# Performance work log

Measured on AMD Instinct MI355X. Metric: run time of the kernel, lower is better.

The kernel has to match this reference:

```python
import jax, jax.numpy as jnp
import numpy as np

B, S, D, H, E, K = 1, 2048, 1024, 16, 8, 2
DK = D // H          # 64 per-head key dim
FF = 4 * D           # 4096 expert hidden
EPS = 1e-5


def rmsnorm(x, scale):
    rms = jnp.sqrt(jnp.mean(x * x, axis=-1, keepdims=True) + EPS)
    return scale * (x / rms)


def setup_inputs() -> dict:
    key = jax.random.key(0)
    ks = jax.random.split(key, 12)
    std = 0.02
    x = jax.random.normal(ks[0], (B, S, D), dtype=jnp.float32)
    # causal mask: masked_fill where mask == 0
    self_attn_mask = jnp.tril(jnp.ones((S, S), dtype=jnp.int32))
    scale_attn = jnp.ones((D,), dtype=jnp.float32)
    scale_ffn = jnp.ones((D,), dtype=jnp.float32)
    # per-head projections, stacked: [H, DK, D] (torch Linear weight layout [out,in])
    Wq = jax.random.normal(ks[1], (H, DK, D), dtype=jnp.float32) * std
    Wk = jax.random.normal(ks[2], (H, DK, D), dtype=jnp.float32) * std
    Wv = jax.random.normal(ks[3], (H, DK, D), dtype=jnp.float32) * std
    Wo = jax.random.normal(ks[4], (D, D), dtype=jnp.float32) * std
    Wg = jax.random.normal(ks[5], (E, D), dtype=jnp.float32) * std   # router gate
    W_in = jax.random.normal(ks[6], (E, FF, D), dtype=jnp.float32) * std   # expert linear
    W_v = jax.random.normal(ks[7], (E, FF, D), dtype=jnp.float32) * std    # expert linear_v
    W_out = jax.random.normal(ks[8], (E, D, FF), dtype=jnp.float32) * std  # expert linear_out
    return {
        'x': x, 'self_attn_mask': self_attn_mask,
        'scale_attn': scale_attn, 'Wq': Wq, 'Wk': Wk, 'Wv': Wv, 'Wo': Wo,
        'scale_ffn': scale_ffn, 'Wg': Wg, 'W_in': W_in, 'W_v': W_v, 'W_out': W_out,
    }


def reference(x, self_attn_mask, scale_attn, Wq, Wk, Wv, Wo, scale_ffn, Wg, W_in, W_v, W_out):
    # --- self attention (pre-RMSNorm) ---
    normed = rmsnorm(x, scale_attn)
    q = jnp.einsum('bsd,hkd->bhsk', normed, Wq)
    k = jnp.einsum('bsd,hkd->bhsk', normed, Wk)
    v = jnp.einsum('bsd,hkd->bhsk', normed, Wv)
    attn = jnp.einsum('bhsk,bhtk->bhst', q, k) / np.sqrt(DK).astype(np.float32)
    attn = jnp.where(self_attn_mask[None, None] == 0, -jnp.inf, attn)
    attn = jax.nn.softmax(attn, axis=-1)
    ctx = jnp.einsum('bhst,bhtk->bhsk', attn, v)
    ctx = ctx.transpose(0, 2, 1, 3).reshape(x.shape[0], x.shape[1], D)  # concat heads
    a1 = ctx @ Wo.T
    x = x + a1
    # --- MoE (pre-RMSNorm) ---
    normed = rmsnorm(x, scale_ffn)
    router_logits = normed @ Wg.T                       # [B,S,E]
    router_probs = jax.nn.softmax(router_logits, axis=-1)
    gate, idx = jax.lax.top_k(router_probs, K)          # [B,S,K]
    gate = gate / jnp.sum(gate, axis=-1, keepdims=True)
    # combine weights per expert: sum of renormalized gates over selected slots
    onehot = (idx[..., None] == jnp.arange(E)).astype(x.dtype)  # [B,S,K,E]
    combine = jnp.sum(gate[..., None] * onehot, axis=2)         # [B,S,E]
    # all-expert dense FFN (faithful to the masked dense loop in torch)
    g = jax.nn.gelu(jnp.einsum('bsd,efd->bsef', normed, W_in), approximate=False)
    val = jnp.einsum('bsd,efd->bsef', normed, W_v)
    eo = jnp.einsum('bsef,edf->bsed', g * val, W_out)           # [B,S,E,D]
    moe_out = jnp.einsum('bse,bsed->bsd', combine, eo)
    out = x + moe_out
    return (out, router_probs)
```

## Files before the change

kernel.cpp:

```cpp
#include <hip/hip_runtime.h>
#include <hip/hip_bf16.h>
#include <math.h>

typedef unsigned int u32;
typedef unsigned short u16;
using bf16x8 = __attribute__((ext_vector_type(8))) short;
using f32x4 = __attribute__((ext_vector_type(4))) float;

#define MFMA_BF16(a, b, c) __builtin_amdgcn_mfma_f32_16x16x32_bf16((a), (b), (c), 0, 0, 0)
#define VMCNT8() asm volatile("s_waitcnt vmcnt(8)" ::: "memory")
#define VMCNT6() asm volatile("s_waitcnt vmcnt(6)" ::: "memory")
#define VMCNT0() asm volatile("s_waitcnt vmcnt(0)" ::: "memory")
#define SBAR() __builtin_amdgcn_s_barrier()
#define SCHED0() __builtin_amdgcn_sched_barrier(0)

constexpr int kS = 2048, kD = 1024, kH = 16, kE = 8, kFF = 4096;
constexpr int kSlotCap = 5120;
constexpr int kMaxTiles = 40;

__device__ __forceinline__ u16 bf16_rne(float f) {
  u32 u = __float_as_uint(f);
  u32 r = (u + 0x7fffu + ((u >> 16) & 1u)) >> 16;
  return (u16)r;
}
__device__ __forceinline__ float bf16_f32(u16 h) { return __uint_as_float(((u32)h) << 16); }
__device__ __forceinline__ u32 pack_hl(float x) {
  u16 hi = bf16_rne(x);
  u16 lo = bf16_rne(x - bf16_f32(hi));
  return ((u32)lo << 16) | (u32)hi;
}
__device__ __forceinline__ void unpack8(const u32* t, bf16x8& h, bf16x8& l) {
#pragma unroll
  for (int j = 0; j < 8; j++) {
    h[j] = (short)(t[j] & 0xffffu);
    l[j] = (short)(t[j] >> 16);
  }
}
__device__ __forceinline__ void gload_lds16(const void* g, void* l) {
  __builtin_amdgcn_global_load_lds((const __attribute__((address_space(1))) u32*)g,
                                   (__attribute__((address_space(3))) u32*)l, 16, 0, 0);
}

__global__ __launch_bounds__(256) void pack_dp3(const float* __restrict__ Wq,
                                                const float* __restrict__ Wk,
                                                const float* __restrict__ Wv,
                                                u16* __restrict__ o) {
  int i = blockIdx.x * 256 + threadIdx.x;
  if (i >= 3072 * 1024) return;
  int n = i >> 10, k = i & 1023;
  float v = (n < 1024) ? Wq[i] : (n < 2048) ? Wk[i - 1024 * 1024] : Wv[i - 2048 * 1024];
  u16 hi = bf16_rne(v);
  u16 lo = bf16_rne(v - bf16_f32(hi));
  size_t b = (size_t)n * 2048 + (size_t)(k >> 5) * 64 + (k & 31);
  o[b] = hi;
  o[b + 32] = lo;
}
__global__ __launch_bounds__(256) void pack_dp1(const float* __restrict__ W,
                                                u16* __restrict__ o, int n_elem) {
  int i = blockIdx.x * 256 + threadIdx.x;
  if (i >= n_elem) return;
  int k = i & 1023, n = i >> 10;
  float v = W[i];
  u16 hi = bf16_rne(v);
  u16 lo = bf16_rne(v - bf16_f32(hi));
  size_t b = (size_t)n * 2048 + (size_t)(k >> 5) * 64 + (k & 31);
  o[b] = hi;
  o[b + 32] = lo;
}
__global__ __launch_bounds__(256) void pack_winv(const float* __restrict__ Wi,
                                                 const float* __restrict__ Wv,
                                                 u16* __restrict__ o) {
  size_t i8 = (size_t)blockIdx.x * 256 + threadIdx.x;
  if (i8 >= (size_t)kE * 8192 * 1024 / 8) return;
  size_t flat = i8 * 8;
  int e = (int)(flat >> 23);
  int r = (int)(flat & ((1u << 23) - 1));
  int n = r >> 10, k = r & 1023;
  const float* src = (n < 4096) ? Wi + ((size_t)e * 4096 + n) * 1024 + k
                                : Wv + ((size_t)e * 4096 + (n - 4096)) * 1024 + k;
  float4 a = *(const float4*)src;
  float4 b = *(const float4*)(src + 4);
  u16 rr[8] = {bf16_rne(a.x), bf16_rne(a.y), bf16_rne(a.z), bf16_rne(a.w),
               bf16_rne(b.x), bf16_rne(b.y), bf16_rne(b.z), bf16_rne(b.w)};
  *(uint4*)(o + flat) = *(uint4*)rr;
}
__global__ __launch_bounds__(256) void pack_bf16_kernel(const float* __restrict__ w,
                                                        u16* __restrict__ o, int n8) {
  int i = blockIdx.x * 256 + threadIdx.x;
  if (i >= n8) return;
  const float4* s = (const float4*)w + (size_t)i * 2;
  float4 a = s[0], b = s[1];
  u16 r[8] = {bf16_rne(a.x), bf16_rne(a.y), bf16_rne(a.z), bf16_rne(a.w),
              bf16_rne(b.x), bf16_rne(b.y), bf16_rne(b.z), bf16_rne(b.w)};
  *(uint4*)(o + (size_t)i * 8) = *(uint4*)r;
}

template <int MODE>
__global__ __launch_bounds__(256) void rmsnorm_kernel(
    const float* __restrict__ x, const float* __restrict__ scale,
    u16* __restrict__ odp, float* __restrict__ of32, u16* __restrict__ ob16) {
  const int s = blockIdx.x;
  const float* row = x + (size_t)s * kD;
  const int c = threadIdx.x * 4;
  float4 v = *(const float4*)(row + c);
  float ss = v.x * v.x + v.y * v.y + v.z * v.z + v.w * v.w;
#pragma unroll
  for (int m = 32; m; m >>= 1) ss += __shfl_xor(ss, m);
  __shared__ float wsum[4];
  if ((threadIdx.x & 63) == 0) wsum[threadIdx.x >> 6] = ss;
  __syncthreads();
  float tot = wsum[0] + wsum[1] + wsum[2] + wsum[3];
  float rinv = 1.0f / sqrtf(tot * (1.0f / kD) + 1e-5f);
  float4 sc = *(const float4*)(scale + c);
  float n[4] = {v.x * rinv * sc.x, v.y * rinv * sc.y, v.z * rinv * sc.z, v.w * rinv * sc.w};
  if (MODE == 0) {
    u16 hv[4], lv[4];
#pragma unroll
    for (int j = 0; j < 4; j++) {
      hv[j] = bf16_rne(n[j]);
      lv[j] = bf16_rne(n[j] - bf16_f32(hv[j]));
    }
    u16* o = odp + (size_t)s * 2048 + (size_t)(c >> 5) * 64 + (c & 31);
    *(uint2*)o = *(uint2*)hv;
    *(uint2*)(o + 32) = *(uint2*)lv;
  } else {
    *(float4*)(of32 + (size_t)s * kD + c) = make_float4(n[0], n[1], n[2], n[3]);
    u16* o = ob16 + (size_t)s * kD + c;
    o[0] = bf16_rne(n[0]); o[1] = bf16_rne(n[1]); o[2] = bf16_rne(n[2]); o[3] = bf16_rne(n[3]);
  }
}

template <int APK, int OUT>
__global__ __launch_bounds__(256) void gemm_dp(
    const void* __restrict__ Av, const u16* __restrict__ Bdp,
    const float* __restrict__ resid, int K,
    u32* __restrict__ oq, u32* __restrict__ ok, u32* __restrict__ ov,
    float* __restrict__ of) {
  __shared__ u16 As[2][128 * 64];
  __shared__ u16 Bs[2][128 * 64];
  const int tid = threadIdx.x, w = tid >> 6, l = tid & 63;
  const int m0 = blockIdx.y * 128, n0 = blockIdx.x * 128;
  const int wr = (w >> 1) * 64, wc = (w & 1) * 64;
  const char* Ab = (const char*)Av;
  const char* Bb = (const char*)Bdp;
  const size_t rowb = (size_t)K * 4;

  size_t asrc[4], bsrc[4];
  int dst[4];
#pragma unroll
  for (int i = 0; i < 4; i++) {
    int fl = i * 256 + tid;
    int row = fl >> 3, cb = fl & 7;
    size_t coff = (size_t)((cb ^ (row & 7)) * 16);
    asrc[i] = (size_t)(m0 + row) * rowb + coff;
    bsrc[i] = (size_t)(n0 + row) * rowb + coff;
    dst[i] = fl * 16;
  }

  f32x4 zero = {0.f, 0.f, 0.f, 0.f};
  f32x4 acc[4][4];
#pragma unroll
  for (int i = 0; i < 4; i++)
#pragma unroll
    for (int j = 0; j < 4; j++) acc[i][j] = zero;

  auto stage = [&](int buf, int s) {
    const char* ap = Ab + (size_t)s * 128;
    const char* bp = Bb + (size_t)s * 128;
#pragma unroll
    for (int i = 0; i < 4; i++) {
      gload_lds16(ap + asrc[i], (char*)&As[buf][0] + dst[i]);
      gload_lds16(bp + bsrc[i], (char*)&Bs[buf][0] + dst[i]);
    }
  };

  const int NS = K / 32;
  stage(0, 0);
  for (int s = 0; s < NS; s++) {
    const int cur = s & 1;
    const bool lastit = (s == NS - 1);
    if (!lastit) stage(cur ^ 1, s + 1);
    if (!lastit) VMCNT8(); else VMCNT0();
    SBAR();
    SCHED0();
    bf16x8 ah[4], al[4], bh[4], bl[4];
    const int g = l >> 4;
    if (APK) {
      const u32* At = (const u32*)&As[cur][0];
#pragma unroll
      for (int mi = 0; mi < 4; mi++) {
        int row = wr + mi * 16 + (l & 15);
        u32 t[8];
        *(uint4*)t = *(const uint4*)&At[row * 32 + (((2 * g) ^ (row & 7)) * 4)];
        *(uint4*)(t + 4) = *(const uint4*)&At[row * 32 + (((2 * g + 1) ^ (row & 7)) * 4)];
        unpack8(t, ah[mi], al[mi]);
      }
    } else {
#pragma unroll
      for (int mi = 0; mi < 4; mi++) {
        int row = wr + mi * 16 + (l & 15);
        ah[mi] = *(const bf16x8*)&As[cur][row * 64 + ((g ^ (row & 7)) * 8)];
        al[mi] = *(const bf16x8*)&As[cur][row * 64 + (((4 + g) ^ (row & 7)) * 8)];
      }
    }
#pragma unroll
    for (int ni = 0; ni < 4; ni++) {
      int row = wc + ni * 16 + (l & 15);
      bh[ni] = *(const bf16x8*)&Bs[cur][row * 64 + ((g ^ (row & 7)) * 8)];
      bl[ni] = *(const bf16x8*)&Bs[cur][row * 64 + (((4 + g) ^ (row & 7)) * 8)];
    }
#pragma unroll
    for (int mi = 0; mi < 4; mi++)
#pragma unroll
      for (int ni = 0; ni < 4; ni++) {
        f32x4 c = acc[mi][ni];
        c = MFMA_BF16(al[mi], bl[ni], c);
        c = MFMA_BF16(al[mi], bh[ni], c);
        c = MFMA_BF16(ah[mi], bl[ni], c);
        c = MFMA_BF16(ah[mi], bh[ni], c);
        acc[mi][ni] = c;
      }
    SCHED0();
    if (!lastit) SBAR();
  }

  if (OUT == 0) {
    u32* dstp;
    int nb;
    if (n0 < 1024) { dstp = oq; nb = n0; }
    else if (n0 < 2048) { dstp = ok; nb = n0 - 1024; }
    else { dstp = ov; nb = n0 - 2048; }
#pragma unroll
    for (int mi = 0; mi < 4; mi++)
#pragma unroll
      for (int ni = 0; ni < 4; ni++)
#pragma unroll
        for (int r = 0; r < 4; r++) {
          int row = m0 + wr + mi * 16 + ((l >> 4) << 2) + r;
          int col = nb + wc + ni * 16 + (l & 15);
          dstp[(size_t)row * 1024 + col] = pack_hl(acc[mi][ni][r]);
        }
  } else {
#pragma unroll
    for (int mi = 0; mi < 4; mi++)
#pragma unroll
      for (int ni = 0; ni < 4; ni++)
#pragma unroll
        for (int r = 0; r < 4; r++) {
          int row = m0 + wr + mi * 16 + ((l >> 4) << 2) + r;
          int col = n0 + wc + ni * 16 + (l & 15);
          of[(size_t)row * 1024 + col] = resid[(size_t)row * 1024 + col] + acc[mi][ni][r];
        }
  }
}

__global__ __launch_bounds__(256) void attn_kernel(
    const u32* __restrict__ Qp, const u32* __restrict__ Kp, const u32* __restrict__ Vp,
    u32* __restrict__ Op) {
  constexpr int LDK = 68;
  __shared__ u32 Ks[64 * LDK];
  __shared__ u32 Vs[64 * LDK];
  __shared__ u32 Ps[64 * LDK];
  const int tid = threadIdx.x, w = tid >> 6, l = tid & 63;
  const int qt = blockIdx.x, hh = blockIdx.y;
  const int q0 = qt * 64, hc = hh * 64;

  bf16x8 qh[2], ql[2];
  {
    const int qrow = q0 + w * 16 + (l & 15);
#pragma unroll
    for (int kk = 0; kk < 2; kk++) {
      u32 t[8];
      const u32* p = Qp + (size_t)qrow * kD + hc + kk * 32 + ((l >> 4) << 3);
      *(uint4*)t = *(const uint4*)p;
      *(uint4*)(t + 4) = *(const uint4*)(p + 4);
      unpack8(t, qh[kk], ql[kk]);
    }
  }
  float mrun[4], lrun[4];
  f32x4 zero = {0.f, 0.f, 0.f, 0.f};
  f32x4 oacc[4];
#pragma unroll
  for (int r = 0; r < 4; r++) { mrun[r] = -3.0e38f; lrun[r] = 0.f; }
#pragma unroll
  for (int vb = 0; vb < 4; vb++) oacc[vb] = zero;

  const int trow = tid >> 2, c0v = (tid & 3) * 16;
  const u32* gKb = Kp + hc + c0v;
  const u32* gVb = Vp + hc + c0v;
  uint4 kr[4], vr[4];
  {
    const u32* gK = gKb + (size_t)trow * kD;
    kr[0] = *(const uint4*)gK; kr[1] = *(const uint4*)(gK + 4);
    kr[2] = *(const uint4*)(gK + 8); kr[3] = *(const uint4*)(gK + 12);
    const u32* gV = gVb + (size_t)trow * kD;
    vr[0] = *(const uint4*)gV; vr[1] = *(const uint4*)(gV + 4);
    vr[2] = *(const uint4*)(gV + 8); vr[3] = *(const uint4*)(gV + 12);
  }

  for (int kt = 0; kt <= qt; kt++) {
    {
      u32* sK = Ks + trow * LDK + c0v;
      *(uint4*)sK = kr[0]; *(uint4*)(sK + 4) = kr[1];
      *(uint4*)(sK + 8) = kr[2]; *(uint4*)(sK + 12) = kr[3];
#pragma unroll
      for (int j = 0; j < 4; j++) {
        Vs[(c0v + j * 4 + 0) * LDK + trow] = vr[j].x;
        Vs[(c0v + j * 4 + 1) * LDK + trow] = vr[j].y;
        Vs[(c0v + j * 4 + 2) * LDK + trow] = vr[j].z;
        Vs[(c0v + j * 4 + 3) * LDK + trow] = vr[j].w;
      }
    }
    __syncthreads();
    if (kt < qt) {
      const u32* gK = gKb + (size_t)((kt + 1) * 64 + trow) * kD;
      kr[0] = *(const uint4*)gK; kr[1] = *(const uint4*)(gK + 4);
      kr[2] = *(const uint4*)(gK + 8); kr[3] = *(const uint4*)(gK + 12);
      const u32* gV = gVb + (size_t)((kt + 1) * 64 + trow) * kD;
      vr[0] = *(const uint4*)gV; vr[1] = *(const uint4*)(gV + 4);
      vr[2] = *(const uint4*)(gV + 8); vr[3] = *(const uint4*)(gV + 12);
    }

    f32x4 sfr[4];
#pragma unroll
    for (int kb = 0; kb < 4; kb++) {
      f32x4 sa = zero;
#pragma unroll
      for (int kk = 0; kk < 2; kk++) {
        u32 t[8];
        bf16x8 kh, kl;
        const u32* p = Ks + (kb * 16 + (l & 15)) * LDK + kk * 32 + ((l >> 4) << 3);
        *(uint4*)t = *(const uint4*)p;
        *(uint4*)(t + 4) = *(const uint4*)(p + 4);
        unpack8(t, kh, kl);
        sa = MFMA_BF16(ql[kk], kl, sa);
        sa = MFMA_BF16(ql[kk], kh, sa);
        sa = MFMA_BF16(qh[kk], kl, sa);
        sa = MFMA_BF16(qh[kk], kh, sa);
      }
      sfr[kb] = sa * 0.125f;
    }
    if (kt == qt) {
#pragma unroll
      for (int kb = 0; kb < 4; kb++) {
        int t = kt * 64 + kb * 16 + (l & 15);
#pragma unroll
        for (int r = 0; r < 4; r++) {
          int qq = q0 + w * 16 + ((l >> 4) << 2) + r;
          if (t > qq) sfr[kb][r] = -3.0e38f;
        }
      }
    }
#pragma unroll
    for (int r = 0; r < 4; r++) {
      float mx = fmaxf(fmaxf(sfr[0][r], sfr[1][r]), fmaxf(sfr[2][r], sfr[3][r]));
#pragma unroll
      for (int mm = 1; mm < 16; mm <<= 1) mx = fmaxf(mx, __shfl_xor(mx, mm));
      float mnew = fmaxf(mrun[r], mx);
      float sf = __expf(mrun[r] - mnew);
      mrun[r] = mnew;
      float rs = 0.f;
#pragma unroll
      for (int kb = 0; kb < 4; kb++) {
        float p = __expf(sfr[kb][r] - mnew);
        sfr[kb][r] = p;
        rs += p;
      }
#pragma unroll
      for (int mm = 1; mm < 16; mm <<= 1) rs += __shfl_xor(rs, mm);
      lrun[r] = lrun[r] * sf + rs;
#pragma unroll
      for (int vb = 0; vb < 4; vb++) oacc[vb][r] *= sf;
    }
#pragma unroll
    for (int kb = 0; kb < 4; kb++)
#pragma unroll
      for (int r = 0; r < 4; r++)
        Ps[(w * 16 + ((l >> 4) << 2) + r) * LDK + kb * 16 + (l & 15)] = pack_hl(sfr[kb][r]);
#pragma unroll
    for (int ks = 0; ks < 2; ks++) {
      bf16x8 ph, pl;
      {
        u32 t[8];
        const u32* pp = Ps + (w * 16 + (l & 15)) * LDK + ks * 32 + ((l >> 4) << 3);
        *(uint4*)t = *(const uint4*)pp;
        *(uint4*)(t + 4) = *(const uint4*)(pp + 4);
        unpack8(t, ph, pl);
      }
#pragma unroll
      for (int vb = 0; vb < 4; vb++) {
        u32 t2[8];
        bf16x8 vh, vl;
        const u32* pv = Vs + (vb * 16 + (l & 15)) * LDK + ks * 32 + ((l >> 4) << 3);
        *(uint4*)t2 = *(const uint4*)pv;
        *(uint4*)(t2 + 4) = *(const uint4*)(pv + 4);
        unpack8(t2, vh, vl);
        f32x4 c = oacc[vb];
        c = MFMA_BF16(pl, vl, c);
        c = MFMA_BF16(pl, vh, c);
        c = MFMA_BF16(ph, vl, c);
        c = MFMA_BF16(ph, vh, c);
        oacc[vb] = c;
      }
    }
    __syncthreads();
  }
#pragma unroll
  for (int vb = 0; vb < 4; vb++)
#pragma unroll
    for (int r = 0; r < 4; r++) {
      float o = oacc[vb][r] / lrun[r];
      int row = q0 + w * 16 + ((l >> 4) << 2) + r;
      int col = hc + vb * 16 + (l & 15);
      Op[(size_t)row * kD + col] = pack_hl(o);
    }
}

__global__ __launch_bounds__(256) void router_kernel(
    const float* __restrict__ normed, const float* __restrict__ Wg,
    float* __restrict__ probs, float* __restrict__ gates,
    int* __restrict__ experts, int* __restrict__ counts) {
  const int w = threadIdx.x >> 6, l = threadIdx.x & 63;
  const int s = blockIdx.x * 4 + w;
  float lg[kE];
  const float* row = normed + (size_t)s * kD;
#pragma unroll
  for (int e = 0; e < kE; e++) {
    const float* wg = Wg + (size_t)e * kD;
    float a = 0.f;
    for (int d = l; d < kD; d += 64) a += row[d] * wg[d];
#pragma unroll
    for (int m = 32; m; m >>= 1) a += __shfl_xor(a, m);
    lg[e] = a;
  }
  if (l == 0) {
    float mx = lg[0];
#pragma unroll
    for (int e = 1; e < kE; e++) mx = fmaxf(mx, lg[e]);
    float p[kE], sum = 0.f;
#pragma unroll
    for (int e = 0; e < kE; e++) { p[e] = __expf(lg[e] - mx); sum += p[e]; }
    float inv = 1.f / sum;
#pragma unroll
    for (int e = 0; e < kE; e++) { p[e] *= inv; probs[(size_t)s * kE + e] = p[e]; }
    int i1 = 0;
#pragma unroll
    for (int e = 1; e < kE; e++) if (lg[e] > lg[i1]) i1 = e;
    int i2 = (i1 == 0) ? 1 : 0;
#pragma unroll
    for (int e = 0; e < kE; e++) if (e != i1 && lg[e] > lg[i2]) i2 = e;
    float den = 1.f / (p[i1] + p[i2]);
    gates[s * 2] = p[i1] * den;
    gates[s * 2 + 1] = p[i2] * den;
    experts[s * 2] = i1;
    experts[s * 2 + 1] = i2;
    atomicAdd(&counts[i1], 1);
    atomicAdd(&counts[i2], 1);
  }
}

__global__ void moe_init(int* counts) {
  if (threadIdx.x < kE) counts[threadIdx.x] = 0;
}
__global__ void moe_scan(const int* __restrict__ counts, int* __restrict__ ebase,
                         int* __restrict__ cursor, int2* __restrict__ tmap) {
  if (threadIdx.x == 0) {
    int acc = 0, t = 0;
    for (int e = 0; e < kE; e++) {
      ebase[e] = acc;
      cursor[e] = acc;
      int nt = (counts[e] + 127) >> 7;
      for (int i = 0; i < nt; i++) tmap[t++] = make_int2(e, i * 128);
      acc += nt << 7;
    }
    ebase[kE] = acc;
    for (; t < kMaxTiles; t++) tmap[t] = make_int2(-1, 0);
  }
}
__global__ void moe_fill(const int* __restrict__ experts, int* __restrict__ cursor,
                         int* __restrict__ slot_list, int* __restrict__ slot_of) {
  int s = blockIdx.x * 256 + threadIdx.x;
  if (s >= kS) return;
  for (int k = 0; k < 2; k++) {
    int e = experts[s * 2 + k];
    int pos = atomicAdd(&cursor[e], 1);
    slot_list[pos] = s;
    slot_of[s * 2 + k] = pos;
  }
}

__global__ __launch_bounds__(256) void moe_mmA(
    const u16* __restrict__ A, const u16* __restrict__ Bg,
    const int* __restrict__ slot_list, const int* __restrict__ counts,
    const int* __restrict__ ebase, const int2* __restrict__ tmap,
    u16* __restrict__ Uraw) {
  int2 tm = tmap[blockIdx.y];
  const int e = tm.x;
  if (e < 0) return;
  const int base = ebase[e], Me = counts[e], m0 = tm.y;
  const int n0 = blockIdx.x * 128;
  __shared__ u16 As[2][128 * 64];
  __shared__ u16 Bs[2][128 * 64];
  const int tid = threadIdx.x, w = tid >> 6, l = tid & 63;
  const int wr = (w >> 1) * 64, wc = (w & 1) * 64;
  const char* Ab = (const char*)A;
  const char* Bb = (const char*)(Bg + ((size_t)e * 8192) * 1024);

  size_t asrc[4], bsrc[4];
  int dst[4];
#pragma unroll
  for (int i = 0; i < 4; i++) {
    int fl = i * 256 + tid;
    int row = fl >> 3, cb = fl & 7;
    size_t coff = (size_t)((cb ^ (row & 7)) * 16);
    int mr = m0 + row;
    if (mr > Me - 1) mr = Me - 1;
    int ar = slot_list[base + mr];
    asrc[i] = (size_t)ar * 2048 + coff;
    bsrc[i] = (size_t)(n0 + row) * 2048 + coff;
    dst[i] = fl * 16;
  }

  f32x4 zero = {0.f, 0.f, 0.f, 0.f};
  f32x4 acc[4][4];
#pragma unroll
  for (int i = 0; i < 4; i++)
#pragma unroll
    for (int j = 0; j < 4; j++) acc[i][j] = zero;

  auto stage = [&](int buf, int s) {
    const size_t so = (size_t)s * 128;
#pragma unroll
    for (int i = 0; i < 4; i++) {
      gload_lds16(Ab + so + asrc[i], (char*)&As[buf][0] + dst[i]);
      gload_lds16(Bb + so + bsrc[i], (char*)&Bs[buf][0] + dst[i]);
    }
  };

  const int NS = kD / 64;
  stage(0, 0);
  for (int s = 0; s < NS; s++) {
    const int cur = s & 1;
    const bool lastit = (s == NS - 1);
    if (!lastit) stage(cur ^ 1, s + 1);
    if (!lastit) VMCNT8(); else VMCNT0();
    SBAR();
    SCHED0();
#pragma unroll
    for (int kk = 0; kk < 2; kk++) {
      const int g = kk * 4 + (l >> 4);
      bf16x8 af[4], bfr[4];
#pragma unroll
      for (int mi = 0; mi < 4; mi++) {
        int row = wr + mi * 16 + (l & 15);
        af[mi] = *(const bf16x8*)&As[cur][row * 64 + ((g ^ (row & 7)) * 8)];
      }
#pragma unroll
      for (int ni = 0; ni < 4; ni++) {
        int row = wc + ni * 16 + (l & 15);
        bfr[ni] = *(const bf16x8*)&Bs[cur][row * 64 + ((g ^ (row & 7)) * 8)];
      }
#pragma unroll
      for (int mi = 0; mi < 4; mi++)
#pragma unroll
        for (int ni = 0; ni < 4; ni++) acc[mi][ni] = MFMA_BF16(af[mi], bfr[ni], acc[mi][ni]);
    }
    SCHED0();
    if (!lastit) SBAR();
  }

#pragma unroll
  for (int mi = 0; mi < 4; mi++)
#pragma unroll
    for (int r = 0; r < 4; r++) {
      int ml = m0 + wr + mi * 16 + ((l >> 4) << 2) + r;
      if (ml >= Me) continue;
      size_t rb = (size_t)(base + ml) * 8192;
#pragma unroll
      for (int ni = 0; ni < 4; ni++) {
        int col = n0 + wc + ni * 16 + (l & 15);
        Uraw[rb + col] = bf16_rne(acc[mi][ni][r]);
      }
    }
}

__global__ __launch_bounds__(256) void gelu_mul(const u16* __restrict__ Uraw,
                                                u16* __restrict__ H) {
  size_t i8 = (size_t)blockIdx.x * 256 + threadIdx.x;
  if (i8 >= (size_t)kSlotCap * kFF / 8) return;
  int row = (int)(i8 >> 9);
  int j8 = ((int)i8 & 511) * 8;
  const u16* up = Uraw + (size_t)row * 8192 + j8;
  uint4 uu = *(const uint4*)up;
  uint4 vv = *(const uint4*)(up + 4096);
  const u16* ue = (const u16*)&uu;
  const u16* ve = (const u16*)&vv;
  u16 o[8];
#pragma unroll
  for (int k = 0; k < 8; k++) {
    float u = bf16_f32(ue[k]), v = bf16_f32(ve[k]);
    float ge = 0.5f * u * (1.0f + erff(u * 0.70710678118654752f));
    o[k] = bf16_rne(ge * v);
  }
  *(uint4*)(H + (size_t)row * kFF + j8) = *(uint4*)o;
}

__global__ __launch_bounds__(256) void moe_mm2(
    const u16* __restrict__ H, const u16* __restrict__ Bg,
    const int* __restrict__ counts, const int* __restrict__ ebase,
    const int2* __restrict__ tmap, float* __restrict__ eo) {
  int2 tm = tmap[blockIdx.y];
  const int e = tm.x;
  if (e < 0) return;
  const int base = ebase[e], Me = counts[e], m0 = tm.y;
  const int n0 = blockIdx.x * 64;
  __shared__ u16 As[2][128 * 64];
  __shared__ u16 Bs[2][64 * 64];
  const int tid = threadIdx.x, w = tid >> 6, l = tid & 63;
  const int wr = (w >> 1) * 64, wc = (w & 1) * 32;
  const char* Ab = (const char*)H;
  const char* Bb = (const char*)(Bg + (size_t)e * kD * kFF);

  size_t asrc[4], bsrc[2];
  int adst[4], bdst[2];
#pragma unroll
  for (int i = 0; i < 4; i++) {
    int fl = i * 256 + tid;
    int row = fl >> 3, cb = fl & 7;
    int mr = m0 + row;
    if (mr > Me - 1) mr = Me - 1;
    asrc[i] = (size_t)(base + mr) * 8192 + (size_t)((cb ^ (row & 7)) * 16);
    adst[i] = fl * 16;
  }
#pragma unroll
  for (int i = 0; i < 2; i++) {
    int fl = i * 256 + tid;
    int row = fl >> 3, cb = fl & 7;
    bsrc[i] = (size_t)(n0 + row) * 8192 + (size_t)((cb ^ (row & 7)) * 16);
    bdst[i] = fl * 16;
  }

  f32x4 zero = {0.f, 0.f, 0.f, 0.f};
  f32x4 acc[4][2];
#pragma unroll
  for (int i = 0; i < 4; i++)
#pragma unroll
    for (int j = 0; j < 2; j++) acc[i][j] = zero;

  auto stage = [&](int buf, int s) {
    const size_t so = (size_t)s * 128;
#pragma unroll
    for (int i = 0; i < 4; i++) gload_lds16(Ab + so + asrc[i], (char*)&As[buf][0] + adst[i]);
#pragma unroll
    for (int i = 0; i < 2; i++) gload_lds16(Bb + so + bsrc[i], (char*)&Bs[buf][0] + bdst[i]);
  };

  const int NS = kFF / 64;
  stage(0, 0);
  for (int s = 0; s < NS; s++) {
    const int cur = s & 1;
    const bool lastit = (s == NS - 1);
    if (!lastit) stage(cur ^ 1, s + 1);
    if (!lastit) VMCNT6(); else VMCNT0();
    SBAR();
    SCHED0();
#pragma unroll
    for (int kk = 0; kk < 2; kk++) {
      const int g = kk * 4 + (l >> 4);
      bf16x8 af[4], bfr[2];
#pragma unroll
      for (int mi = 0; mi < 4; mi++) {
        int row = wr + mi * 16 + (l & 15);
        af[mi] = *(const bf16x8*)&As[cur][row * 64 + ((g ^ (row & 7)) * 8)];
      }
#pragma unroll
      for (int ni = 0; ni < 2; ni++) {
        int row = wc + ni * 16 + (l & 15);
        bfr[ni] = *(const bf16x8*)&Bs[cur][row * 64 + ((g ^ (row & 7)) * 8)];
      }
#pragma unroll
      for (int mi = 0; mi < 4; mi++)
#pragma unroll
        for (int ni = 0; ni < 2; ni++) acc[mi][ni] = MFMA_BF16(af[mi], bfr[ni], acc[mi][ni]);
    }
    SCHED0();
    if (!lastit) SBAR();
  }

#pragma unroll
  for (int mi = 0; mi < 4; mi++)
#pragma unroll
    for (int r = 0; r < 4; r++) {
      int ml = m0 + wr + mi * 16 + ((l >> 4) << 2) + r;
      if (ml >= Me) continue;
      size_t rb = (size_t)(base + ml) * kD;
#pragma unroll
      for (int ni = 0; ni < 2; ni++) {
        int col = n0 + wc + ni * 16 + (l & 15);
        eo[rb + col] = acc[mi][ni][r];
      }
    }
}

__global__ __launch_bounds__(256) void combine_kernel(
    const float* __restrict__ h, const float* __restrict__ eo,
    const float* __restrict__ gates, const int* __restrict__ slot_of,
    float* __restrict__ out) {
  const int s = blockIdx.x;
  const float g0 = gates[s * 2], g1 = gates[s * 2 + 1];
  const int p0 = slot_of[s * 2], p1 = slot_of[s * 2 + 1];
  const int c = threadIdx.x * 4;
  float4 hv = *(const float4*)(h + (size_t)s * kD + c);
  float4 e0 = *(const float4*)(eo + (size_t)p0 * kD + c);
  float4 e1 = *(const float4*)(eo + (size_t)p1 * kD + c);
  float4 o;
  o.x = hv.x + g0 * e0.x + g1 * e1.x;
  o.y = hv.y + g0 * e0.y + g1 * e1.y;
  o.z = hv.z + g0 * e0.z + g1 * e1.z;
  o.w = hv.w + g0 * e0.w + g1 * e1.w;
  *(float4*)(out + (size_t)s * kD + c) = o;
}

extern "C" void kernel_launch(void* const* d_in, const int* in_sizes, int n_in,
                              void* d_out, int out_size, void* d_ws, size_t ws_size,
                              hipStream_t stream) {
  (void)in_sizes; (void)n_in; (void)out_size; (void)ws_size;
  const float* x = (const float*)d_in[0];
  const float* scale_attn = (const float*)d_in[2];
  const float* Wq = (const float*)d_in[3];
  const float* Wk = (const float*)d_in[4];
  const float* Wv = (const float*)d_in[5];
  const float* Wo = (const float*)d_in[6];
  const float* scale_ffn = (const float*)d_in[7];
  const float* Wg = (const float*)d_in[8];
  const float* W_in = (const float*)d_in[9];
  const float* W_vv = (const float*)d_in[10];
  const float* W_out = (const float*)d_in[11];
  float* out = (float*)d_out;
  float* probs = out + (size_t)kS * kD;

  char* wsb = (char*)d_ws;
  size_t off = 0;
  auto alloc = [&](size_t bytes) -> void* {
    void* p = wsb + off;
    off += (bytes + 255) & ~(size_t)255;
    return p;
  };
  const size_t SDu = (size_t)kS * kD;
  u16* Uraw = (u16*)wsb;
  u16* normA_dp = (u16*)alloc(SDu * 4);
  u32* qpk = (u32*)alloc(SDu * 4);
  u32* kpk = (u32*)alloc(SDu * 4);
  u32* vpk = (u32*)alloc(SDu * 4);
  u32* ctxpk = (u32*)alloc(SDu * 4);
  u16* Wqkv_dp = (u16*)alloc((size_t)3072 * 2048 * 2);
  u16* Wo_dp = (u16*)alloc((size_t)1024 * 2048 * 2);
  float* normFf = (float*)alloc(SDu * 4);
  float* eo = (float*)alloc((size_t)kSlotCap * kD * 4);
  float* h = (float*)alloc(SDu * 4);
  u16* normFb = (u16*)alloc(SDu * 2);
  u16* Winv_bf = (u16*)alloc((size_t)kE * 8192 * 1024 * 2);
  u16* Wout_bf = (u16*)alloc((size_t)kE * kD * kFF * 2);
  u16* H = (u16*)alloc((size_t)kSlotCap * kFF * 2);
  float* gates = (float*)alloc(kS * 2 * 4);
  int* experts = (int*)alloc(kS * 2 * 4);
  int* slot_of = (int*)alloc(kS * 2 * 4);
  int* slot_list = (int*)alloc(kSlotCap * 4);
  int* counts = (int*)alloc(64);
  int* ebase = (int*)alloc(64);
  int* cursor = (int*)alloc(64);
  int2* tmap = (int2*)alloc(kMaxTiles * 8);

  pack_dp3<<<(3072 * 1024) / 256, 256, 0, stream>>>(Wq, Wk, Wv, Wqkv_dp);
  pack_dp1<<<(1024 * 1024) / 256, 256, 0, stream>>>(Wo, Wo_dp, 1024 * 1024);
  pack_winv<<<(int)((size_t)kE * 8192 * 1024 / 8 / 256), 256, 0, stream>>>(W_in, W_vv, Winv_bf);
  const int n8o = (int)((size_t)kE * kD * kFF / 8);
  pack_bf16_kernel<<<(n8o + 255) / 256, 256, 0, stream>>>(W_out, Wout_bf, n8o);

  rmsnorm_kernel<0><<<kS, 256, 0, stream>>>(x, scale_attn, normA_dp, nullptr, nullptr);
  gemm_dp<0, 0><<<dim3(3072 / 128, kS / 128), 256, 0, stream>>>(
      normA_dp, Wqkv_dp, nullptr, kD, qpk, kpk, vpk, nullptr);
  attn_kernel<<<dim3(kS / 64, kH), 256, 0, stream>>>(qpk, kpk, vpk, ctxpk);
  gemm_dp<1, 1><<<dim3(1024 / 128, kS / 128), 256, 0, stream>>>(
      ctxpk, Wo_dp, x, kD, nullptr, nullptr, nullptr, h);

  rmsnorm_kernel<1><<<kS, 256, 0, stream>>>(h, scale_ffn, nullptr, normFf, normFb);
  moe_init<<<1, 64, 0, stream>>>(counts);
  router_kernel<<<kS / 4, 256, 0, stream>>>(normFf, Wg, probs, gates, experts, counts);
  moe_scan<<<1, 64, 0, stream>>>(counts, ebase, cursor, tmap);
  moe_fill<<<kS / 256, 256, 0, stream>>>(experts, cursor, slot_list, slot_of);

  moe_mmA<<<dim3(8192 / 128, kMaxTiles), 256, 0, stream>>>(
      normFb, Winv_bf, slot_list, counts, ebase, tmap, Uraw);
  gelu_mul<<<(int)((size_t)kSlotCap * kFF / 8 / 256), 256, 0, stream>>>(Uraw, H);
  moe_mm2<<<dim3(kD / 64, kMaxTiles), 256, 0, stream>>>(
      H, Wout_bf, counts, ebase, tmap, eo);

  combine_kernel<<<kS, 256, 0, stream>>>(h, eo, gates, slot_of, out);
}
```

Baseline: 719.6 us.

## Split causal attention over KV chunks and merge partials in a new kernel

Splits each query tile's causal KV loop into chunks of 8 key tiles, so long query tiles are handled by up to 4 blocks instead of one. This balances work across the grid and raises block count from 512 to 1280. Each block writes unnormalized fp32 partial output plus its running max and sum, and a new merge kernel combines them with log-sum-exp weighting. The cost is an extra launch and extra global traffic for the partials.

```diff
diff --git a/kernel.cpp b/kernel.cpp
--- a/kernel.cpp
+++ b/kernel.cpp
@@ -17,6 +17,7 @@
 constexpr int kS = 2048, kD = 1024, kH = 16, kE = 8, kFF = 4096;
 constexpr int kSlotCap = 5120;
 constexpr int kMaxTiles = 40;
+constexpr int kChunk = 8;
 
 __device__ __forceinline__ u16 bf16_rne(float f) {
   u32 u = __float_as_uint(f);
@@ -256,14 +257,21 @@
 
 __global__ __launch_bounds__(256) void attn_kernel(
     const u32* __restrict__ Qp, const u32* __restrict__ Kp, const u32* __restrict__ Vp,
-    u32* __restrict__ Op) {
+    float* __restrict__ Opart, float* __restrict__ mpart, float* __restrict__ lpart) {
   constexpr int LDK = 68;
   __shared__ u32 Ks[64 * LDK];
   __shared__ u32 Vs[64 * LDK];
   __shared__ u32 Ps[64 * LDK];
   const int tid = threadIdx.x, w = tid >> 6, l = tid & 63;
-  const int qt = blockIdx.x, hh = blockIdx.y;
+  int b = blockIdx.x, qt, c;
+  if (b < 8) { qt = b; c = 0; }
+  else if (b < 24) { qt = 8 + ((b - 8) >> 1); c = (b - 8) & 1; }
+  else if (b < 48) { qt = 16 + (b - 24) / 3; c = (b - 24) % 3; }
+  else { qt = 24 + ((b - 48) >> 2); c = (b - 48) & 3; }
+  const int hh = blockIdx.y;
   const int q0 = qt * 64, hc = hh * 64;
+  const int kt0 = c * kChunk;
+  const int kt1 = min(kt0 + kChunk, qt + 1);
 
   bf16x8 qh[2], ql[2];
   {
@@ -290,15 +298,15 @@
   const u32* gVb = Vp + hc + c0v;
   uint4 kr[4], vr[4];
   {
-    const u32* gK = gKb + (size_t)trow * kD;
+    const u32* gK = gKb + (size_t)(kt0 * 64 + trow) * kD;
     kr[0] = *(const uint4*)gK; kr[1] = *(const uint4*)(gK + 4);
     kr[2] = *(const uint4*)(gK + 8); kr[3] = *(const uint4*)(gK + 12);
-    const u32* gV = gVb + (size_t)trow * kD;
+    const u32* gV = gVb + (size_t)(kt0 * 64 + trow) * kD;
     vr[0] = *(const uint4*)gV; vr[1] = *(const uint4*)(gV + 4);
     vr[2] = *(const uint4*)(gV + 8); vr[3] = *(const uint4*)(gV + 12);
   }
 
-  for (int kt = 0; kt <= qt; kt++) {
+  for (int kt = kt0; kt < kt1; kt++) {
     {
       u32* sK = Ks + trow * LDK + c0v;
       *(uint4*)sK = kr[0]; *(uint4*)(sK + 4) = kr[1];
@@ -312,7 +320,7 @@
       }
     }
     __syncthreads();
-    if (kt < qt) {
+    if (kt + 1 < kt1) {
       const u32* gK = gKb + (size_t)((kt + 1) * 64 + trow) * kD;
       kr[0] = *(const uint4*)gK; kr[1] = *(const uint4*)(gK + 4);
       kr[2] = *(const uint4*)(gK + 8); kr[3] = *(const uint4*)(gK + 12);
@@ -395,25 +403,67 @@
         *(uint4*)t2 = *(const uint4*)pv;
         *(uint4*)(t2 + 4) = *(const uint4*)(pv + 4);
         unpack8(t2, vh, vl);
-        f32x4 c = oacc[vb];
-        c = MFMA_BF16(pl, vl, c);
-        c = MFMA_BF16(pl, vh, c);
-        c = MFMA_BF16(ph, vl, c);
-        c = MFMA_BF16(ph, vh, c);
-        oacc[vb] = c;
+        f32x4 cc = oacc[vb];
+        cc = MFMA_BF16(pl, vl, cc);
+        cc = MFMA_BF16(pl, vh, cc);
+        cc = MFMA_BF16(ph, vl, cc);
+        cc = MFMA_BF16(ph, vh, cc);
+        oacc[vb] = cc;
       }
     }
     __syncthreads();
   }
+
+  const int p = (qt * 16 + hh) * 4 + c;
+  float* Po = Opart + (size_t)p * 4096;
 #pragma unroll
   for (int vb = 0; vb < 4; vb++)
 #pragma unroll
     for (int r = 0; r < 4; r++) {
-      float o = oacc[vb][r] / lrun[r];
-      int row = q0 + w * 16 + ((l >> 4) << 2) + r;
-      int col = hc + vb * 16 + (l & 15);
-      Op[(size_t)row * kD + col] = pack_hl(o);
-    }
+      int rl = w * 16 + ((l >> 4) << 2) + r;
+      int cl = vb * 16 + (l & 15);
+      Po[rl * 64 + cl] = oacc[vb][r];
+    }
+  if ((l & 15) == 0) {
+#pragma unroll
+    for (int r = 0; r < 4; r++) {
+      int rl = w * 16 + ((l >> 4) << 2) + r;
+      mpart[p * 64 + rl] = mrun[r];
+      lpart[p * 64 + rl] = lrun[r];
+    }
+  }
+}
+
+__global__ __launch_bounds__(256) void attn_merge(
+    const float* __restrict__ Opart, const float* __restrict__ mpart,
+    const float* __restrict__ lpart, u32* __restrict__ Op) {
+  const int qt = blockIdx.x, hh = blockIdx.y;
+  const int nch = (qt + kChunk) >> 3;
+  const int t = threadIdx.x;
+  const int row = t >> 2;
+  const int c0 = (t & 3) * 16;
+  const int pbase = (qt * 16 + hh) * 4;
+  float M = -3.0e38f;
+  for (int c = 0; c < nch; c++) M = fmaxf(M, mpart[(pbase + c) * 64 + row]);
+  float den = 0.f;
+  float acc[16];
+#pragma unroll
+  for (int j = 0; j < 16; j++) acc[j] = 0.f;
+  for (int c = 0; c < nch; c++) {
+    float wgt = __expf(mpart[(pbase + c) * 64 + row] - M);
+    den += wgt * lpart[(pbase + c) * 64 + row];
+    const float* po = Opart + (size_t)(pbase + c) * 4096 + row * 64 + c0;
+#pragma unroll
+    for (int j = 0; j < 16; j += 4) {
+      float4 v = *(const float4*)(po + j);
+      acc[j] += wgt * v.x; acc[j + 1] += wgt * v.y;
+      acc[j + 2] += wgt * v.z; acc[j + 3] += wgt * v.w;
+    }
+  }
+  float inv = 1.f / den;
+  u32* dst = Op + (size_t)(qt * 64 + row) * kD + hh * 64 + c0;
+#pragma unroll
+  for (int j = 0; j < 16; j++) dst[j] = pack_hl(acc[j] * inv);
 }
 
 __global__ __launch_bounds__(256) void router_kernel(
@@ -762,6 +812,9 @@
   u16* Winv_bf = (u16*)alloc((size_t)kE * 8192 * 1024 * 2);
   u16* Wout_bf = (u16*)alloc((size_t)kE * kD * kFF * 2);
   u16* H = (u16*)alloc((size_t)kSlotCap * kFF * 2);
+  float* Opart = (float*)alloc((size_t)2048 * 4096 * 4);
+  float* mpart = (float*)alloc((size_t)2048 * 64 * 4);
+  float* lpart = (float*)alloc((size_t)2048 * 64 * 4);
   float* gates = (float*)alloc(kS * 2 * 4);
   int* experts = (int*)alloc(kS * 2 * 4);
   int* slot_of = (int*)alloc(kS * 2 * 4);
@@ -780,7 +833,8 @@
   rmsnorm_kernel<0><<<kS, 256, 0, stream>>>(x, scale_attn, normA_dp, nullptr, nullptr);
   gemm_dp<0, 0><<<dim3(3072 / 128, kS / 128), 256, 0, stream>>>(
       normA_dp, Wqkv_dp, nullptr, kD, qpk, kpk, vpk, nullptr);
-  attn_kernel<<<dim3(kS / 64, kH), 256, 0, stream>>>(qpk, kpk, vpk, ctxpk);
+  attn_kernel<<<dim3(80, kH), 256, 0, stream>>>(qpk, kpk, vpk, Opart, mpart, lpart);
+  attn_merge<<<dim3(kS / 64, kH), 256, 0, stream>>>(Opart, mpart, lpart, ctxpk);
   gemm_dp<1, 1><<<dim3(1024 / 128, kS / 128), 256, 0, stream>>>(
       ctxpk, Wo_dp, x, kD, nullptr, nullptr, nullptr, h);
 
```

Result: faster. 678.2 us (-5.8%).
